# Kernel optimization log

Measured on AMD Instinct MI355X. Metric: run time of the kernel, lower is better.

## Reference

```python
import jax, jax.numpy as jnp
import numpy as np

H = 16  # num_heads

def setup_inputs() -> dict:
    key = jax.random.key(0)
    k_x, k_q, k_k, k_v, k_o = jax.random.split(key, 5)
    B, L, D = 2, 2048, 1024
    s = 0.02
    return {
        "x": jax.random.normal(k_x, (B, L, D), dtype=jnp.float32),
        "Wq": jax.random.normal(k_q, (D, D), dtype=jnp.float32) * s,
        "Wk": jax.random.normal(k_k, (D, D), dtype=jnp.float32) * s,
        "Wv": jax.random.normal(k_v, (D, D), dtype=jnp.float32) * s,
        "Wo": jax.random.normal(k_o, (D, D), dtype=jnp.float32) * s,
    }

def reference(x, Wq, Wk, Wv, Wo):
    B, L, D = x.shape
    hd = D // H
    scale = hd ** -0.5
    # projections: nn.Linear applies x @ W.T; with random weights we use x @ W
    q = (x @ Wq).reshape(B, L, H, hd).transpose(0, 2, 1, 3)  # [B,H,L,hd]
    k = (x @ Wk).reshape(B, L, H, hd).transpose(0, 2, 1, 3)
    v = (x @ Wv).reshape(B, L, H, hd).transpose(0, 2, 1, 3)
    attn = jnp.einsum("bhqd,bhkd->bhqk", q, k) * scale  # [B,H,L,L]
    causal = jnp.tril(jnp.ones((L, L), dtype=bool))
    attn = jnp.where(causal, attn, jnp.float32(-jnp.inf))
    attn = jax.nn.softmax(attn, axis=-1)
    out = jnp.einsum("bhqk,bhkd->bhqd", attn, v)  # [B,H,L,hd]
    out = out.transpose(0, 2, 1, 3).reshape(B, L, D)
    return out @ Wo
```

## Files before the change

kernel.cpp:

```cpp
#include <hip/hip_runtime.h>
#include <cstdint>
#include <cstddef>

typedef __attribute__((ext_vector_type(8))) __bf16 bf16x8;
typedef __attribute__((ext_vector_type(4))) float f32x4;

__device__ __forceinline__ unsigned short f2bf(float x) {
    unsigned int u = __float_as_uint(x);
    u += 0x7fffu + ((u >> 16) & 1u);
    return (unsigned short)(u >> 16);
}

__device__ __forceinline__ ushort4 pack4bf(float a, float b, float c, float d) {
    union { ushort4 v; __bf16 e[4]; } u;
    u.e[0] = (__bf16)a; u.e[1] = (__bf16)b; u.e[2] = (__bf16)c; u.e[3] = (__bf16)d;
    return u.v;
}

#if defined(__has_builtin)
#if __has_builtin(__builtin_amdgcn_exp2f)
#define EXP2(x) __builtin_amdgcn_exp2f(x)
#else
#define EXP2(x) exp2f(x)
#endif
#else
#define EXP2(x) exp2f(x)
#endif

typedef const __attribute__((address_space(1))) void* gptr_t;
typedef __attribute__((address_space(3))) void* lptr_t;
__device__ __forceinline__ void gload_lds16(const void* g, void* l) {
    __builtin_amdgcn_global_load_lds((gptr_t)g, (lptr_t)l, 16, 0, 0);
}

__global__ __launch_bounds__(256) void cast_x_kernel(const float* __restrict__ x,
                                                     unsigned short* __restrict__ out) {
    int i = blockIdx.x * 256 + threadIdx.x;
    float4 v = ((const float4*)x)[i];
    ushort4 o;
    o.x = f2bf(v.x); o.y = f2bf(v.y); o.z = f2bf(v.z); o.w = f2bf(v.w);
    ((ushort4*)out)[i] = o;
}

__global__ __launch_bounds__(256) void transpose4_kernel(const float* __restrict__ W0,
                                                         const float* __restrict__ W1,
                                                         const float* __restrict__ W2,
                                                         const float* __restrict__ W3,
                                                         unsigned short* __restrict__ T0,
                                                         unsigned short* __restrict__ T1,
                                                         unsigned short* __restrict__ T2,
                                                         unsigned short* __restrict__ T3,
                                                         float s0) {
    __shared__ float Ts[64][65];
    const int D = 1024;
    const int m = blockIdx.z;
    const float* W = (m == 0) ? W0 : (m == 1) ? W1 : (m == 2) ? W2 : W3;
    unsigned short* T = (m == 0) ? T0 : (m == 1) ? T1 : (m == 2) ? T2 : T3;
    const float scale = (m == 0) ? s0 : 1.0f;
    const int kt = blockIdx.y * 64, nt = blockIdx.x * 64;
    const int tid = threadIdx.x;

    {
        const int r = tid >> 2, cs = (tid & 3) * 16;
#pragma unroll
        for (int j = 0; j < 16; j += 4) {
            f32x4 v = *(const f32x4*)&W[(size_t)(kt + r) * D + nt + cs + j];
#pragma unroll
            for (int e = 0; e < 4; ++e) Ts[r][cs + j + e] = v[e];
        }
    }
    __syncthreads();
    {
        const int n = tid >> 2, ks = (tid & 3) * 16;
        union { bf16x8 v[2]; __bf16 e[16]; } cv;
#pragma unroll
        for (int j = 0; j < 16; ++j) cv.e[j] = (__bf16)(Ts[ks + j][n] * scale);
        *(bf16x8*)&T[(size_t)(nt + n) * D + kt + ks] = cv.v[0];
        *(bf16x8*)&T[(size_t)(nt + n) * D + kt + ks + 8] = cv.v[1];
    }
}

template <int OUTBF, int VT>
__global__ __launch_bounds__(256) void gemm_bt(const unsigned short* __restrict__ A,
                                               const unsigned short* __restrict__ Bt,
                                               void* __restrict__ Cout,
                                               unsigned short* __restrict__ Vt,
                                               int M, int N, int K, int lda, int ldc,
                                               int nbx) {
    __shared__ __align__(16) unsigned short Au[128 * 64];
    __shared__ __align__(16) unsigned short Bs[128 * 64];
    const int tid = threadIdx.x;
    const int w = tid >> 6;
    const int lane = tid & 63;

    const int nwg = gridDim.x;
    const int q8 = nwg >> 3;
    const int orig = blockIdx.x;
    const int newlin = (orig & 7) * q8 + (orig >> 3);
    const int by = newlin / nbx;
    const int bx = newlin - by * nbx;
    const int m0 = by * 128;
    const int n0 = bx * 128;
    const int wr = w >> 1, wc = w & 1;

    f32x4 acc[4][4];
#pragma unroll
    for (int i = 0; i < 4; ++i)
#pragma unroll
        for (int j = 0; j < 4; ++j) acc[i][j] = f32x4{0.f, 0.f, 0.f, 0.f};

    const int srow = tid >> 3;
    const int sch = (tid & 7) ^ (srow & 7);

    const int fq = lane & 15, fg = lane >> 4;
    const int xa0 = ((fg ^ (fq & 7)) << 3);
    const int xa1 = (((fg ^ 4) ^ (fq & 7)) << 3);

    for (int kt = 0; kt < K; kt += 64) {
#pragma unroll
        for (int p = 0; p < 4; ++p) {
            gload_lds16(A + (size_t)(m0 + p * 32 + srow) * lda + kt + sch * 8,
                        &Au[(p * 256 + w * 64) * 8]);
            gload_lds16(Bt + (size_t)(n0 + p * 32 + srow) * K + kt + sch * 8,
                        &Bs[(p * 256 + w * 64) * 8]);
        }
        __syncthreads();

        bf16x8 af[4], bfr[4];
#pragma unroll
        for (int m = 0; m < 4; ++m)
            af[m] = *(const bf16x8*)&Au[(wr * 64 + m * 16 + fq) * 64 + xa0];
#pragma unroll
        for (int n = 0; n < 4; ++n)
            bfr[n] = *(const bf16x8*)&Bs[(wc * 64 + n * 16 + fq) * 64 + xa0];
#pragma unroll
        for (int m = 0; m < 4; ++m)
#pragma unroll
            for (int n = 0; n < 4; ++n)
                acc[m][n] = __builtin_amdgcn_mfma_f32_16x16x32_bf16(af[m], bfr[n], acc[m][n], 0, 0, 0);
#pragma unroll
        for (int m = 0; m < 4; ++m)
            af[m] = *(const bf16x8*)&Au[(wr * 64 + m * 16 + fq) * 64 + xa1];
#pragma unroll
        for (int n = 0; n < 4; ++n)
            bfr[n] = *(const bf16x8*)&Bs[(wc * 64 + n * 16 + fq) * 64 + xa1];
#pragma unroll
        for (int m = 0; m < 4; ++m)
#pragma unroll
            for (int n = 0; n < 4; ++n)
                acc[m][n] = __builtin_amdgcn_mfma_f32_16x16x32_bf16(af[m], bfr[n], acc[m][n], 0, 0, 0);
        __syncthreads();
    }

    const int crow = (lane >> 4) * 4;
    const int ccol = lane & 15;

    if constexpr (VT) {
        if (n0 >= 2048) {
            __shared__ __align__(16) unsigned short Tw[4][32 * 72];
            const int bb = m0 >> 11;
            const int h = ((n0 - 2048) >> 6) + wc;
            const int kvbase = (m0 & 2047) + wr * 64;
            unsigned short* vdst = Vt + (size_t)((bb * 16 + h) * 64) * 2048 + kvbase;
#pragma unroll
            for (int pass = 0; pass < 2; ++pass) {
#pragma unroll
                for (int m = 0; m < 4; ++m)
#pragma unroll
                    for (int nn = 0; nn < 2; ++nn) {
                        int n = pass * 2 + nn;
                        int c = nn * 16 + ccol;
                        *(ushort4*)&Tw[w][c * 72 + m * 16 + crow] =
                            pack4bf(acc[m][n][0], acc[m][n][1], acc[m][n][2], acc[m][n][3]);
                    }
                asm volatile("" ::: "memory");
                const int d_loc = lane >> 1;
                const int kvh = (lane & 1) * 32;
                unsigned short* dst = vdst + (size_t)(pass * 32 + d_loc) * 2048 + kvh;
#pragma unroll
                for (int i = 0; i < 4; ++i) {
                    bf16x8 v = *(const bf16x8*)&Tw[w][d_loc * 72 + kvh + i * 8];
                    *(bf16x8*)&dst[i * 8] = v;
                }
                asm volatile("" ::: "memory");
            }
            return;
        }
    }

#pragma unroll
    for (int m = 0; m < 4; ++m) {
#pragma unroll
        for (int n = 0; n < 4; ++n) {
            int r0 = m0 + wr * 64 + m * 16 + crow;
            int c0 = n0 + wc * 64 + n * 16 + ccol;
#pragma unroll
            for (int j = 0; j < 4; ++j) {
                if (OUTBF)
                    ((unsigned short*)Cout)[(size_t)(r0 + j) * ldc + c0] = f2bf(acc[m][n][j]);
                else
                    ((float*)Cout)[(size_t)(r0 + j) * ldc + c0] = acc[m][n][j];
            }
        }
    }
}

__global__ __launch_bounds__(256) void flash_kernel(unsigned short* __restrict__ QKV,
                                                    const unsigned short* __restrict__ Vt) {
    __shared__ __align__(16) unsigned short Ks[2][64 * 64];
    __shared__ __align__(16) unsigned short Vs[64 * 64];
    __shared__ __align__(16) unsigned short Ps[4][16 * 72];

    const int tid = threadIdx.x;
    const int w = tid >> 6;
    const int lane = tid & 63;
    const int bh = blockIdx.x;
    const int b = bh >> 4, h = bh & 15;
    const int rowbase = b * 2048;
    const int hd0 = h * 64;
    const int S = 3072;

    const int qi = lane & 15;
    const int g = lane >> 4;
    const int x0 = ((g ^ (qi & 7)) << 3);
    const int x1 = (((g ^ 4) ^ (qi & 7)) << 3);

    const int qblk = (31 - (int)blockIdx.y) * 64;
    const int q0 = qblk + w * 16;
    const int nt = qblk / 64 + 1;
    const int q_rel = w * 16 + qi;

    const unsigned short* gK[2];
    const unsigned short* gV[2];
#pragma unroll
    for (int p = 0; p < 2; ++p) {
        int row = p * 32 + w * 8 + (lane >> 3);
        int ch = (lane & 7) ^ (row & 7);
        gK[p] = QKV + (size_t)(rowbase + row) * S + 1024 + hd0 + ch * 8;
        gV[p] = Vt + (size_t)(bh * 64 + row) * 2048 + ch * 8;
    }

#define STAGE_K(buf)                                            \
    do {                                                        \
        gload_lds16(gK[0], &Ks[buf][w * 512]);                  \
        gload_lds16(gK[1], &Ks[buf][2048 + w * 512]);           \
        gK[0] += 64 * S; gK[1] += 64 * S;                       \
    } while (0)
#define STAGE_V()                                               \
    do {                                                        \
        gload_lds16(gV[0], &Vs[w * 512]);                       \
        gload_lds16(gV[1], &Vs[2048 + w * 512]);                \
        gV[0] += 64; gV[1] += 64;                               \
    } while (0)

    bf16x8 qf[2];
#pragma unroll
    for (int st = 0; st < 2; ++st)
        qf[st] = *(const bf16x8*)(QKV + (size_t)(rowbase + q0 + qi) * S + hd0 +
                                  st * 32 + g * 8);

    float m_prev = -1e30f, lsum = 0.f;
    f32x4 oacc[4];
#pragma unroll
    for (int n = 0; n < 4; ++n) oacc[n] = f32x4{0.f, 0.f, 0.f, 0.f};

    STAGE_K(0);
    STAGE_V();
    if (nt > 1) STAGE_K(1);
    __syncthreads();

    for (int t = 0; t < nt; ++t) {
        const int cur = t & 1;
        const unsigned short* Kc = Ks[cur];

        f32x4 sacc[4];
        __builtin_amdgcn_s_setprio(1);
#pragma unroll
        for (int n = 0; n < 4; ++n) {
            bf16x8 k0 = *(const bf16x8*)&Kc[(n * 16 + qi) * 64 + x0];
            bf16x8 k1 = *(const bf16x8*)&Kc[(n * 16 + qi) * 64 + x1];
            f32x4 c = f32x4{0.f, 0.f, 0.f, 0.f};
            c = __builtin_amdgcn_mfma_f32_16x16x32_bf16(k0, qf[0], c, 0, 0, 0);
            c = __builtin_amdgcn_mfma_f32_16x16x32_bf16(k1, qf[1], c, 0, 0, 0);
            sacc[n] = c;
        }
        __builtin_amdgcn_s_setprio(0);

        const bool diag = (t == nt - 1);
        if (diag) {
#pragma unroll
            for (int n = 0; n < 4; ++n)
#pragma unroll
                for (int j = 0; j < 4; ++j)
                    if (n * 16 + g * 4 + j > q_rel) sacc[n][j] = -1e30f;
        }
        float tmax = -1e30f;
#pragma unroll
        for (int n = 0; n < 4; ++n) {
            float a = fmaxf(fmaxf(sacc[n][0], sacc[n][1]), fmaxf(sacc[n][2], sacc[n][3]));
            tmax = fmaxf(tmax, a);
        }
        const bool defer = __all(tmax - m_prev <= 8.0f);
        float mcur = m_prev;
        if (!defer) {
            tmax = fmaxf(tmax, __shfl_xor(tmax, 16));
            tmax = fmaxf(tmax, __shfl_xor(tmax, 32));
            mcur = fmaxf(m_prev, tmax);
            float alpha = EXP2(m_prev - mcur);
            lsum *= alpha;
#pragma unroll
            for (int n = 0; n < 4; ++n)
#pragma unroll
                for (int j = 0; j < 4; ++j) oacc[n][j] *= alpha;
            m_prev = mcur;
        }

        float psum = 0.f;
#pragma unroll
        for (int n = 0; n < 4; ++n) {
            float p0 = EXP2(sacc[n][0] - mcur);
            float p1 = EXP2(sacc[n][1] - mcur);
            float p2 = EXP2(sacc[n][2] - mcur);
            float p3 = EXP2(sacc[n][3] - mcur);
            psum += (p0 + p1) + (p2 + p3);
            *(ushort4*)&Ps[w][qi * 72 + n * 16 + g * 4] = pack4bf(p0, p1, p2, p3);
        }
        lsum += psum;

        asm volatile("" ::: "memory");

        __syncthreads();

        __builtin_amdgcn_s_setprio(1);
#pragma unroll
        for (int st = 0; st < 2; ++st) {
            bf16x8 ptf = *(const bf16x8*)&Ps[w][qi * 72 + st * 32 + g * 8];
            const int xo = st ? x1 : x0;
#pragma unroll
            for (int n = 0; n < 4; ++n) {
                bf16x8 vfr = *(const bf16x8*)&Vs[(n * 16 + qi) * 64 + xo];
                oacc[n] = __builtin_amdgcn_mfma_f32_16x16x32_bf16(vfr, ptf, oacc[n], 0, 0, 0);
            }
        }
        __builtin_amdgcn_s_setprio(0);

        __syncthreads();
        if (t + 1 < nt) STAGE_V();
        if (t + 2 < nt) STAGE_K(cur);
    }
#undef STAGE_K
#undef STAGE_V

    {
        lsum += __shfl_xor(lsum, 16);
        lsum += __shfl_xor(lsum, 32);
        float inv = 1.0f / lsum;
#pragma unroll
        for (int n = 0; n < 4; ++n)
            *(ushort4*)&Ps[w][qi * 72 + n * 16 + g * 4] =
                pack4bf(oacc[n][0] * inv, oacc[n][1] * inv, oacc[n][2] * inv, oacc[n][3] * inv);
        asm volatile("" ::: "memory");
        const int r = lane >> 2;
        const int cs = (lane & 3) * 16;
        bf16x8 o0 = *(const bf16x8*)&Ps[w][r * 72 + cs];
        bf16x8 o1 = *(const bf16x8*)&Ps[w][r * 72 + cs + 8];
        *(bf16x8*)&QKV[(size_t)(rowbase + q0 + r) * S + hd0 + cs] = o0;
        *(bf16x8*)&QKV[(size_t)(rowbase + q0 + r) * S + hd0 + cs + 8] = o1;
    }
}

extern "C" void kernel_launch(void* const* d_in, const int* in_sizes, int n_in,
                              void* d_out, int out_size, void* d_ws, size_t ws_size,
                              hipStream_t stream) {
    const float* x  = (const float*)d_in[0];
    const float* Wq = (const float*)d_in[1];
    const float* Wk = (const float*)d_in[2];
    const float* Wv = (const float*)d_in[3];
    const float* Wo = (const float*)d_in[4];
    float* out = (float*)d_out;

    const int WN = 1024 * 1024;
    const int XN = 4096 * 1024;

    unsigned short* ws   = (unsigned short*)d_ws;
    unsigned short* Wqkv = ws;
    unsigned short* Wot  = Wqkv + 3 * WN;
    unsigned short* QKV  = Wot + WN;
    unsigned short* Xbf  = (unsigned short*)d_out;
    unsigned short* Vt   = Xbf + XN;

    cast_x_kernel<<<XN / 1024, 256, 0, stream>>>(x, Xbf);

    transpose4_kernel<<<dim3(16, 16, 4), 256, 0, stream>>>(
        Wq, Wk, Wv, Wo, Wqkv, Wqkv + WN, Wqkv + 2 * WN, Wot, 0.125f * 1.4426950408889634f);

    gemm_bt<1, 1><<<24 * 32, 256, 0, stream>>>(
        Xbf, Wqkv, QKV, Vt, 4096, 3072, 1024, 1024, 3072, 24);

    flash_kernel<<<dim3(32, 32), 256, 0, stream>>>(QKV, Vt);

    gemm_bt<0, 0><<<8 * 32, 256, 0, stream>>>(
        QKV, Wot, out, nullptr, 4096, 1024, 1024, 3072, 1024, 8);
}
```

Before: 105.2 us.

## Software-pipeline flash attention QK^T with previous softmax/PV; narrow output GEMM tiles

The flash attention loop now computes S for tile t while running softmax and PV for tile t-1, with the causal mask applied only in an epilogue for the final diagonal tile. The goal is to overlap MFMA work on QK^T with the exp/max latency of softmax. Separately, gemm_bt gets a template parameter for N-tile width, and the output projection uses 128x64 tiles, launching 512 workgroups instead of 256 to fill more CUs. The trade-offs are extra registers for the saved score tile and less reuse of the A tile in the narrower GEMM.

```diff
diff --git a/kernel.cpp b/kernel.cpp
--- a/kernel.cpp
+++ b/kernel.cpp
@@ -80,15 +80,16 @@
     }
 }
 
-template <int OUTBF, int VT>
+template <int OUTBF, int VT, int NBF>
 __global__ __launch_bounds__(256) void gemm_bt(const unsigned short* __restrict__ A,
                                                const unsigned short* __restrict__ Bt,
                                                void* __restrict__ Cout,
                                                unsigned short* __restrict__ Vt,
                                                int M, int N, int K, int lda, int ldc,
                                                int nbx) {
+    static_assert(!VT || NBF == 4, "VT path requires NBF=4");
     __shared__ __align__(16) unsigned short Au[128 * 64];
-    __shared__ __align__(16) unsigned short Bs[128 * 64];
+    __shared__ __align__(16) unsigned short Bs[NBF * 32 * 64];
     const int tid = threadIdx.x;
     const int w = tid >> 6;
     const int lane = tid & 63;
@@ -100,14 +101,14 @@
     const int by = newlin / nbx;
     const int bx = newlin - by * nbx;
     const int m0 = by * 128;
-    const int n0 = bx * 128;
+    const int n0 = bx * (NBF * 32);
     const int wr = w >> 1, wc = w & 1;
 
-    f32x4 acc[4][4];
+    f32x4 acc[4][NBF];
 #pragma unroll
     for (int i = 0; i < 4; ++i)
 #pragma unroll
-        for (int j = 0; j < 4; ++j) acc[i][j] = f32x4{0.f, 0.f, 0.f, 0.f};
+        for (int j = 0; j < NBF; ++j) acc[i][j] = f32x4{0.f, 0.f, 0.f, 0.f};
 
     const int srow = tid >> 3;
     const int sch = (tid & 7) ^ (srow & 7);
@@ -118,36 +119,37 @@
 
     for (int kt = 0; kt < K; kt += 64) {
 #pragma unroll
-        for (int p = 0; p < 4; ++p) {
+        for (int p = 0; p < 4; ++p)
             gload_lds16(A + (size_t)(m0 + p * 32 + srow) * lda + kt + sch * 8,
                         &Au[(p * 256 + w * 64) * 8]);
+#pragma unroll
+        for (int p = 0; p < NBF; ++p)
             gload_lds16(Bt + (size_t)(n0 + p * 32 + srow) * K + kt + sch * 8,
                         &Bs[(p * 256 + w * 64) * 8]);
-        }
         __syncthreads();
 
-        bf16x8 af[4], bfr[4];
+        bf16x8 af[4], bfr[NBF];
 #pragma unroll
         for (int m = 0; m < 4; ++m)
             af[m] = *(const bf16x8*)&Au[(wr * 64 + m * 16 + fq) * 64 + xa0];
 #pragma unroll
-        for (int n = 0; n < 4; ++n)
-            bfr[n] = *(const bf16x8*)&Bs[(wc * 64 + n * 16 + fq) * 64 + xa0];
+        for (int n = 0; n < NBF; ++n)
+            bfr[n] = *(const bf16x8*)&Bs[(wc * (NBF * 16) + n * 16 + fq) * 64 + xa0];
 #pragma unroll
         for (int m = 0; m < 4; ++m)
 #pragma unroll
-            for (int n = 0; n < 4; ++n)
+            for (int n = 0; n < NBF; ++n)
                 acc[m][n] = __builtin_amdgcn_mfma_f32_16x16x32_bf16(af[m], bfr[n], acc[m][n], 0, 0, 0);
 #pragma unroll
         for (int m = 0; m < 4; ++m)
             af[m] = *(const bf16x8*)&Au[(wr * 64 + m * 16 + fq) * 64 + xa1];
 #pragma unroll
-        for (int n = 0; n < 4; ++n)
-            bfr[n] = *(const bf16x8*)&Bs[(wc * 64 + n * 16 + fq) * 64 + xa1];
+        for (int n = 0; n < NBF; ++n)
+            bfr[n] = *(const bf16x8*)&Bs[(wc * (NBF * 16) + n * 16 + fq) * 64 + xa1];
 #pragma unroll
         for (int m = 0; m < 4; ++m)
 #pragma unroll
-            for (int n = 0; n < 4; ++n)
+            for (int n = 0; n < NBF; ++n)
                 acc[m][n] = __builtin_amdgcn_mfma_f32_16x16x32_bf16(af[m], bfr[n], acc[m][n], 0, 0, 0);
         __syncthreads();
     }
@@ -191,9 +193,9 @@
 #pragma unroll
     for (int m = 0; m < 4; ++m) {
 #pragma unroll
-        for (int n = 0; n < 4; ++n) {
+        for (int n = 0; n < NBF; ++n) {
             int r0 = m0 + wr * 64 + m * 16 + crow;
-            int c0 = n0 + wc * 64 + n * 16 + ccol;
+            int c0 = n0 + wc * (NBF * 16) + n * 16 + ccol;
 #pragma unroll
             for (int j = 0; j < 4; ++j) {
                 if (OUTBF)
@@ -263,17 +265,66 @@
     f32x4 oacc[4];
 #pragma unroll
     for (int n = 0; n < 4; ++n) oacc[n] = f32x4{0.f, 0.f, 0.f, 0.f};
+    f32x4 sprev[4], snew[4];
 
     STAGE_K(0);
-    STAGE_V();
     if (nt > 1) STAGE_K(1);
     __syncthreads();
 
+#define SOFTMAX(sp)                                                            \
+    do {                                                                       \
+        float tmax = m_prev;                                                   \
+        _Pragma("unroll")                                                      \
+        for (int n = 0; n < 4; ++n) {                                          \
+            tmax = fmaxf(fmaxf(tmax, sp[n][0]), sp[n][1]);                     \
+            tmax = fmaxf(fmaxf(tmax, sp[n][2]), sp[n][3]);                     \
+        }                                                                      \
+        const bool defer = __all(tmax - m_prev <= 8.0f);                       \
+        float mcur = m_prev;                                                   \
+        if (!defer) {                                                          \
+            tmax = fmaxf(tmax, __shfl_xor(tmax, 16));                          \
+            tmax = fmaxf(tmax, __shfl_xor(tmax, 32));                          \
+            mcur = tmax;                                                       \
+            float alpha = EXP2(m_prev - mcur);                                 \
+            lsum *= alpha;                                                     \
+            _Pragma("unroll")                                                  \
+            for (int n = 0; n < 4; ++n)                                        \
+                _Pragma("unroll")                                              \
+                for (int j = 0; j < 4; ++j) oacc[n][j] *= alpha;               \
+            m_prev = mcur;                                                     \
+        }                                                                      \
+        float psum = 0.f;                                                      \
+        _Pragma("unroll")                                                      \
+        for (int n = 0; n < 4; ++n) {                                          \
+            float p0 = EXP2(sp[n][0] - mcur);                                  \
+            float p1 = EXP2(sp[n][1] - mcur);                                  \
+            float p2 = EXP2(sp[n][2] - mcur);                                  \
+            float p3 = EXP2(sp[n][3] - mcur);                                  \
+            psum += (p0 + p1) + (p2 + p3);                                     \
+            *(ushort4*)&Ps[w][qi * 72 + n * 16 + g * 4] = pack4bf(p0, p1, p2, p3); \
+        }                                                                      \
+        lsum += psum;                                                          \
+    } while (0)
+
+#define PV_STEP()                                                              \
+    do {                                                                       \
+        __builtin_amdgcn_s_setprio(1);                                         \
+        _Pragma("unroll")                                                      \
+        for (int st = 0; st < 2; ++st) {                                       \
+            bf16x8 ptf = *(const bf16x8*)&Ps[w][qi * 72 + st * 32 + g * 8];    \
+            const int xo = st ? x1 : x0;                                       \
+            _Pragma("unroll")                                                  \
+            for (int n = 0; n < 4; ++n) {                                      \
+                bf16x8 vfr = *(const bf16x8*)&Vs[(n * 16 + qi) * 64 + xo];     \
+                oacc[n] = __builtin_amdgcn_mfma_f32_16x16x32_bf16(vfr, ptf, oacc[n], 0, 0, 0); \
+            }                                                                  \
+        }                                                                      \
+        __builtin_amdgcn_s_setprio(0);                                         \
+    } while (0)
+
     for (int t = 0; t < nt; ++t) {
-        const int cur = t & 1;
-        const unsigned short* Kc = Ks[cur];
-
-        f32x4 sacc[4];
+        const unsigned short* Kc = Ks[t & 1];
+
         __builtin_amdgcn_s_setprio(1);
 #pragma unroll
         for (int n = 0; n < 4; ++n) {
@@ -282,74 +333,38 @@
             f32x4 c = f32x4{0.f, 0.f, 0.f, 0.f};
             c = __builtin_amdgcn_mfma_f32_16x16x32_bf16(k0, qf[0], c, 0, 0, 0);
             c = __builtin_amdgcn_mfma_f32_16x16x32_bf16(k1, qf[1], c, 0, 0, 0);
-            sacc[n] = c;
+            snew[n] = c;
         }
         __builtin_amdgcn_s_setprio(0);
 
-        const bool diag = (t == nt - 1);
-        if (diag) {
-#pragma unroll
-            for (int n = 0; n < 4; ++n)
-#pragma unroll
-                for (int j = 0; j < 4; ++j)
-                    if (n * 16 + g * 4 + j > q_rel) sacc[n][j] = -1e30f;
-        }
-        float tmax = -1e30f;
-#pragma unroll
-        for (int n = 0; n < 4; ++n) {
-            float a = fmaxf(fmaxf(sacc[n][0], sacc[n][1]), fmaxf(sacc[n][2], sacc[n][3]));
-            tmax = fmaxf(tmax, a);
-        }
-        const bool defer = __all(tmax - m_prev <= 8.0f);
-        float mcur = m_prev;
-        if (!defer) {
-            tmax = fmaxf(tmax, __shfl_xor(tmax, 16));
-            tmax = fmaxf(tmax, __shfl_xor(tmax, 32));
-            mcur = fmaxf(m_prev, tmax);
-            float alpha = EXP2(m_prev - mcur);
-            lsum *= alpha;
-#pragma unroll
-            for (int n = 0; n < 4; ++n)
-#pragma unroll
-                for (int j = 0; j < 4; ++j) oacc[n][j] *= alpha;
-            m_prev = mcur;
-        }
-
-        float psum = 0.f;
-#pragma unroll
-        for (int n = 0; n < 4; ++n) {
-            float p0 = EXP2(sacc[n][0] - mcur);
-            float p1 = EXP2(sacc[n][1] - mcur);
-            float p2 = EXP2(sacc[n][2] - mcur);
-            float p3 = EXP2(sacc[n][3] - mcur);
-            psum += (p0 + p1) + (p2 + p3);
-            *(ushort4*)&Ps[w][qi * 72 + n * 16 + g * 4] = pack4bf(p0, p1, p2, p3);
-        }
-        lsum += psum;
+        if (t > 0) SOFTMAX(sprev);
 
         asm volatile("" ::: "memory");
-
         __syncthreads();
 
-        __builtin_amdgcn_s_setprio(1);
-#pragma unroll
-        for (int st = 0; st < 2; ++st) {
-            bf16x8 ptf = *(const bf16x8*)&Ps[w][qi * 72 + st * 32 + g * 8];
-            const int xo = st ? x1 : x0;
-#pragma unroll
-            for (int n = 0; n < 4; ++n) {
-                bf16x8 vfr = *(const bf16x8*)&Vs[(n * 16 + qi) * 64 + xo];
-                oacc[n] = __builtin_amdgcn_mfma_f32_16x16x32_bf16(vfr, ptf, oacc[n], 0, 0, 0);
-            }
-        }
-        __builtin_amdgcn_s_setprio(0);
+        if (t > 0) PV_STEP();
 
         __syncthreads();
-        if (t + 1 < nt) STAGE_V();
-        if (t + 2 < nt) STAGE_K(cur);
+        STAGE_V();
+        if (t + 2 < nt) STAGE_K(t & 1);
+
+#pragma unroll
+        for (int n = 0; n < 4; ++n) sprev[n] = snew[n];
     }
 #undef STAGE_K
 #undef STAGE_V
+
+    __syncthreads();
+#pragma unroll
+    for (int n = 0; n < 4; ++n)
+#pragma unroll
+        for (int j = 0; j < 4; ++j)
+            if (n * 16 + g * 4 + j > q_rel) sprev[n][j] = -1e30f;
+    SOFTMAX(sprev);
+    asm volatile("" ::: "memory");
+    PV_STEP();
+#undef SOFTMAX
+#undef PV_STEP
 
     {
         lsum += __shfl_xor(lsum, 16);
@@ -394,11 +409,11 @@
     transpose4_kernel<<<dim3(16, 16, 4), 256, 0, stream>>>(
         Wq, Wk, Wv, Wo, Wqkv, Wqkv + WN, Wqkv + 2 * WN, Wot, 0.125f * 1.4426950408889634f);
 
-    gemm_bt<1, 1><<<24 * 32, 256, 0, stream>>>(
+    gemm_bt<1, 1, 4><<<24 * 32, 256, 0, stream>>>(
         Xbf, Wqkv, QKV, Vt, 4096, 3072, 1024, 1024, 3072, 24);
 
     flash_kernel<<<dim3(32, 32), 256, 0, stream>>>(QKV, Vt);
 
-    gemm_bt<0, 0><<<8 * 32, 256, 0, stream>>>(
-        QKV, Wot, out, nullptr, 4096, 1024, 1024, 3072, 1024, 8);
-}
+    gemm_bt<0, 0, 2><<<16 * 32, 256, 0, stream>>>(
+        QKV, Wot, out, nullptr, 4096, 1024, 1024, 3072, 1024, 16);
+}
```

Result: faster. 100.7 us (-4.2%).
